# Performance work log

Hardware: AMD Instinct MI355X
Metric: run time of the kernel (lower is better)

Reference implementation:

```python
import jax, jax.numpy as jnp
import numpy as np
from itertools import product

# Static config
B, H, W, C = 16, 64, 64, 256
WIN = 8            # window size (square)
SHIFT = 4          # cyclic shift
NH = 8             # heads
HD = C // NH       # head dim
N = WIN * WIN      # tokens per window
HIDDEN = 1024


def _rel_pos_index():
    coords = np.stack(np.meshgrid(np.arange(WIN), np.arange(WIN), indexing='ij'))  # (2,w,w)
    flat = coords.reshape(2, -1)                                   # (2,N)
    rel = flat[:, :, None] - flat[:, None, :]                      # (2,N,N)
    rel = rel.transpose(1, 2, 0).astype(np.int64)
    rel[..., 0] += WIN - 1
    rel[..., 1] += WIN - 1
    rel[..., 0] *= 2 * WIN - 1
    return rel.sum(-1)                                             # (N,N)


def _shift_mask():
    # additive mask (nW, N, N) with -100 across shift boundaries (generate_mask)
    img = np.zeros((H, W), dtype=np.float32)
    slices = [(slice(0, -WIN), slice(-WIN, -SHIFT), slice(-SHIFT, None))] * 2
    cnt = 0
    for sx, sy in product(*slices):
        img[sx, sy] = cnt
        cnt += 1
    mw = img.reshape(H // WIN, WIN, W // WIN, WIN).transpose(0, 2, 1, 3).reshape(-1, N)  # (nW,N)
    diff = mw[:, None, :] - mw[:, :, None]
    return np.where(diff != 0, -100.0, 0.0).astype(np.float32)     # (nW,N,N)


REL_IDX = jnp.asarray(_rel_pos_index())
MASK = jnp.asarray(_shift_mask())


def _layernorm(x, scale, bias, eps=1e-5):
    mu = jnp.mean(x, axis=-1, keepdims=True)
    var = jnp.mean(jnp.square(x - mu), axis=-1, keepdims=True)
    return (x - mu) * jax.lax.rsqrt(var + eps) * scale + bias


def setup_inputs() -> dict:
    key = jax.random.key(0)
    ks = jax.random.split(key, 8)
    s = lambda fan_in: 1.0 / np.sqrt(fan_in)
    return {
        'x': jax.random.normal(ks[0], (B, H, W, C), jnp.float32),
        'ln1_scale': jnp.ones((C,), jnp.float32),
        'ln1_bias': jnp.zeros((C,), jnp.float32),
        'qkv_w': jax.random.normal(ks[1], (3 * C, C), jnp.float32) * s(C),
        'qkv_b': jnp.zeros((3 * C,), jnp.float32),
        'proj_w': jax.random.normal(ks[2], (C, C), jnp.float32) * s(C),
        'proj_b': jnp.zeros((C,), jnp.float32),
        'rel_bias': jax.random.normal(ks[3], ((2 * WIN - 1) ** 2, NH), jnp.float32) * 0.02,
        'ln2_scale': jnp.ones((C,), jnp.float32),
        'ln2_bias': jnp.zeros((C,), jnp.float32),
        'mlp_w1': jax.random.normal(ks[4], (HIDDEN, C), jnp.float32) * s(C),
        'mlp_b1': jnp.zeros((HIDDEN,), jnp.float32),
        'mlp_w2': jax.random.normal(ks[5], (C, HIDDEN), jnp.float32) * s(HIDDEN),
        'mlp_b2': jnp.zeros((C,), jnp.float32),
    }


def reference(x, ln1_scale, ln1_bias, qkv_w, qkv_b, proj_w, proj_b, rel_bias,
              ln2_scale, ln2_bias, mlp_w1, mlp_b1, mlp_w2, mlp_b2):
    nWh, nWw = H // WIN, W // WIN
    nW = nWh * nWw

    shortcut = x
    h = _layernorm(x, ln1_scale, ln1_bias)
    # cyclic shift
    h = jnp.roll(h, shift=(-SHIFT, -SHIFT), axis=(1, 2))
    # window partition -> (B*nW, N, C)
    h = h.reshape(B, nWh, WIN, nWw, WIN, C).transpose(0, 1, 3, 2, 4, 5).reshape(B * nW, N, C)

    # qkv
    qkv = h @ qkv_w.T + qkv_b                                # (B*nW, N, 3C)
    qkv = qkv.reshape(B * nW, N, 3, NH, HD)
    q, k, v = qkv[:, :, 0], qkv[:, :, 1], qkv[:, :, 2]       # (B*nW, N, NH, HD)

    scale = 1.0 / np.sqrt(HD)
    attn = jnp.einsum('bnhd,bmhd->bhnm', q * scale, k)       # (B*nW, NH, N, N)
    attn = attn + rel_bias[REL_IDX].transpose(2, 0, 1)[None]  # rel-pos bias (NH,N,N)
    attn = attn.reshape(B, nW, NH, N, N) + MASK[None, :, None]
    attn = jax.nn.softmax(attn.reshape(B * nW, NH, N, N), axis=-1)

    out = jnp.einsum('bhnm,bmhd->bnhd', attn, v).reshape(B * nW, N, C)
    out = out @ proj_w.T + proj_b

    # window reverse + reverse shift
    out = out.reshape(B, nWh, nWw, WIN, WIN, C).transpose(0, 1, 3, 2, 4, 5).reshape(B, H, W, C)
    out = jnp.roll(out, shift=(SHIFT, SHIFT), axis=(1, 2))

    x = shortcut + out
    # MLP
    h2 = _layernorm(x, ln2_scale, ln2_bias)
    h2 = jax.nn.gelu(h2 @ mlp_w1.T + mlp_b1, approximate=False) @ mlp_w2.T + mlp_b2
    return x + h2
```

## Files before the change

kernel.cpp:

```cpp
#include <hip/hip_runtime.h>
#include <hip/hip_bf16.h>
#include <math.h>

#define AS1 __attribute__((address_space(1)))
#define AS3 __attribute__((address_space(3)))

typedef __bf16  bf16x8 __attribute__((ext_vector_type(8)));
typedef float   f32x4  __attribute__((ext_vector_type(4)));
typedef __hip_bfloat16 bf16;

__device__ __forceinline__ void gload_lds16(const void* g, void* l) {
  __builtin_amdgcn_global_load_lds((const AS1 void*)g, (AS3 void*)l, 16, 0, 0);
}

__global__ __launch_bounds__(256) void k_conv_weights(
    const float* __restrict__ qkvw, const float* __restrict__ projw,
    const float* __restrict__ w1, const float* __restrict__ w2,
    bf16* __restrict__ dst)
{
  int i = blockIdx.x * 256 + threadIdx.x;
  float v;
  if (i < 196608)       v = qkvw[i];
  else if (i < 262144)  v = projw[i - 196608];
  else if (i < 524288)  v = w1[i - 262144];
  else                  v = w2[i - 524288];
  dst[i] = __float2bfloat16(v);
}

__global__ __launch_bounds__(256) void k_build_btab(
    const float* __restrict__ rel_bias, float* __restrict__ btab)
{
  int i = blockIdx.x * 256 + threadIdx.x;
  int h = i >> 12, r = i & 4095, n = r >> 6, m = r & 63;
  int idx = ((n >> 3) - (m >> 3) + 7) * 15 + ((n & 7) - (m & 7) + 7);
  btab[i] = rel_bias[idx * 8 + h];
}

__global__ __launch_bounds__(256) void k_ln1_window(
    const float* __restrict__ x, const float* __restrict__ sc,
    const float* __restrict__ bi, bf16* __restrict__ hout)
{
  int t = blockIdx.x * 4 + (threadIdx.x >> 6);
  int lane = threadIdx.x & 63;
  int win = t >> 6, nn = t & 63;
  int b = win >> 6, ww = win & 63;
  int ry = ((ww >> 3) << 3) + (nn >> 3);
  int rx = ((ww & 7) << 3) + (nn & 7);
  int sy = (ry + 4) & 63, sx = (rx + 4) & 63;
  const float* src = x + ((size_t)(((b << 6) + sy) << 6) + sx) * 256;
  f32x4 v = *(const f32x4*)(src + lane * 4);
  float s = v[0] + v[1] + v[2] + v[3];
  #pragma unroll
  for (int o = 1; o < 64; o <<= 1) s += __shfl_xor(s, o);
  float mu = s * (1.0f / 256.0f);
  float d0 = v[0]-mu, d1 = v[1]-mu, d2 = v[2]-mu, d3 = v[3]-mu;
  float q = d0*d0 + d1*d1 + d2*d2 + d3*d3;
  #pragma unroll
  for (int o = 1; o < 64; o <<= 1) q += __shfl_xor(q, o);
  float rstd = rsqrtf(q * (1.0f / 256.0f) + 1e-5f);
  int c = lane * 4;
  union { bf16 h[4]; uint2 u; } pk;
  pk.h[0] = __float2bfloat16(d0 * rstd * sc[c+0] + bi[c+0]);
  pk.h[1] = __float2bfloat16(d1 * rstd * sc[c+1] + bi[c+1]);
  pk.h[2] = __float2bfloat16(d2 * rstd * sc[c+2] + bi[c+2]);
  pk.h[3] = __float2bfloat16(d3 * rstd * sc[c+3] + bi[c+3]);
  *(uint2*)(hout + (size_t)t * 256 + c) = pk.u;
}

template<int EPI>
__global__ __launch_bounds__(256, 2) void k_pipe_ar(
    const bf16* __restrict__ A, const bf16* __restrict__ Bw,
    const float* __restrict__ bias,
    float* __restrict__ Cf, bf16* __restrict__ Cb,
    const float* __restrict__ resid,
    const float* __restrict__ ln2s, const float* __restrict__ ln2b,
    bf16* __restrict__ ln2out, int N)
{
  __shared__ __align__(16) char lds[65536 + 10240];

  const int tid = threadIdx.x;
  const int wid = tid >> 6;
  const int lane = tid & 63;
  const int l15 = lane & 15, lh = lane >> 4;
  const int rowBase = blockIdx.x * 128 + wid * 32;
  const int NC = N >> 5;
  char* scr = lds + 65536 + wid * 2560;

  auto stage = [&](int c) {
    char* dst = lds + (c & 3) * 16384;
    const char* srcB = (const char*)Bw + (size_t)c * 32 * 512;
    #pragma unroll
    for (int i = 0; i < 4; ++i) {
      int off = (i * 256 + tid) * 16;
      int r = off >> 9, cb = off & 511;
      int csw = cb ^ ((r & 7) << 4);
      gload_lds16(srcB + (size_t)r * 512 + csw, dst + off);
    }
  };

  bf16x8 af[2][8];
  {
    const bf16* a0 = A + (size_t)(rowBase + l15) * 256 + lh * 8;
    #pragma unroll
    for (int kk = 0; kk < 8; ++kk) {
      af[0][kk] = *(const bf16x8*)(a0 + kk * 32);
      af[1][kk] = *(const bf16x8*)(a0 + 4096 + kk * 32);
    }
  }

  auto remap = [&](int row) -> size_t {
    int win = row >> 6, nn = row & 63;
    int b = win >> 6, ww = win & 63;
    int ry = ((ww >> 3) << 3) + (nn >> 3);
    int rx = ((ww & 7) << 3) + (nn & 7);
    int fy = (ry + 4) & 63, fx = (rx + 4) & 63;
    return ((size_t)(((b << 6) + fy) << 6) + fx) * 256;
  };
  size_t ra0 = 0, ra1 = 0;
  size_t rbA, rbB;
  if (EPI == 2) {
    ra0 = remap(rowBase + l15);
    ra1 = remap(rowBase + 16 + l15);
    rbA = remap(rowBase + (lane >> 2));
    rbB = remap(rowBase + 16 + (lane >> 2));
  } else {
    rbA = (size_t)(rowBase + (lane >> 2)) * N;
    rbB = rbA + (size_t)16 * N;
  }

  const int cl = lh * 4;
  f32x4 bc0 = *(const f32x4*)(bias + cl);
  f32x4 bc1 = *(const f32x4*)(bias + cl + 16);
  f32x4 rc00, rc10, rc01, rc11;
  if (EPI == 2) {
    rc00 = *(const f32x4*)(resid + ra0 + cl);
    rc10 = *(const f32x4*)(resid + ra1 + cl);
    rc01 = *(const f32x4*)(resid + ra0 + cl + 16);
    rc11 = *(const f32x4*)(resid + ra1 + cl + 16);
  }
  stage(0); stage(1); stage(2);
  asm volatile("s_waitcnt vmcnt(8)" ::: "memory");
  __builtin_amdgcn_sched_barrier(0);

  float s0 = 0.f, q0 = 0.f, s1 = 0.f, q1 = 0.f;

  for (int c = 0; c < NC; ++c) {
    __builtin_amdgcn_s_barrier();
    __builtin_amdgcn_sched_barrier(0);

    f32x4 bn0, bn1, rn00, rn10, rn01, rn11;
    if (c + 1 < NC) {
      const int ncl = (c + 1) * 32 + cl;
      bn0 = *(const f32x4*)(bias + ncl);
      bn1 = *(const f32x4*)(bias + ncl + 16);
      if (EPI == 2) {
        rn00 = *(const f32x4*)(resid + ra0 + ncl);
        rn10 = *(const f32x4*)(resid + ra1 + ncl);
        rn01 = *(const f32x4*)(resid + ra0 + ncl + 16);
        rn11 = *(const f32x4*)(resid + ra1 + ncl + 16);
      }
    }
    if (c + 3 < NC) stage(c + 3);

    const char* buf = lds + (c & 3) * 16384;
    const int xr = (l15 & 7) << 4;
    const int base0 = l15 * 512;
    f32x4 a00 = (f32x4){0.f,0.f,0.f,0.f};
    f32x4 a10 = (f32x4){0.f,0.f,0.f,0.f};
    f32x4 a01 = (f32x4){0.f,0.f,0.f,0.f};
    f32x4 a11 = (f32x4){0.f,0.f,0.f,0.f};
    #pragma unroll
    for (int kk = 0; kk < 8; ++kk) {
      const int ko = (kk * 64 + lh * 16) ^ xr;
      bf16x8 b0 = *(const bf16x8*)(buf + base0 + ko);
      bf16x8 b1 = *(const bf16x8*)(buf + base0 + 8192 + ko);
      a00 = __builtin_amdgcn_mfma_f32_16x16x32_bf16(b0, af[0][kk], a00, 0, 0, 0);
      a10 = __builtin_amdgcn_mfma_f32_16x16x32_bf16(b0, af[1][kk], a10, 0, 0, 0);
      a01 = __builtin_amdgcn_mfma_f32_16x16x32_bf16(b1, af[0][kk], a01, 0, 0, 0);
      a11 = __builtin_amdgcn_mfma_f32_16x16x32_bf16(b1, af[1][kk], a11, 0, 0, 0);
    }

    const int cbs = c * 32 + (lane & 3) * 8;
    if (EPI == 0) {
      union { bf16 h[4]; uint2 u; } p00, p01, p10, p11;
      #pragma unroll
      for (int j = 0; j < 4; ++j) {
        p00.h[j] = __float2bfloat16(a00[j] + bc0[j]);
        p01.h[j] = __float2bfloat16(a01[j] + bc1[j]);
        p10.h[j] = __float2bfloat16(a10[j] + bc0[j]);
        p11.h[j] = __float2bfloat16(a11[j] + bc1[j]);
      }
      *(uint2*)(scr + l15 * 80 + lh * 8)            = p00.u;
      *(uint2*)(scr + l15 * 80 + 32 + lh * 8)       = p01.u;
      *(uint2*)(scr + (16 + l15) * 80 + lh * 8)     = p10.u;
      *(uint2*)(scr + (16 + l15) * 80 + 32 + lh * 8)= p11.u;
      uint4 r0 = *(const uint4*)(scr + (lane >> 2) * 80 + (lane & 3) * 16);
      uint4 r1 = *(const uint4*)(scr + (16 + (lane >> 2)) * 80 + (lane & 3) * 16);
      *(uint4*)(Cb + rbA + cbs) = r0;
      *(uint4*)(Cb + rbB + cbs) = r1;
    } else {
      const int colb0 = c * 32 + cl, colb1 = colb0 + 16;
      f32x4 o00, o10, o01, o11;
      #pragma unroll
      for (int j = 0; j < 4; ++j) {
        o00[j] = a00[j] + bc0[j] + rc00[j];
        o10[j] = a10[j] + bc0[j] + rc10[j];
        o01[j] = a01[j] + bc1[j] + rc01[j];
        o11[j] = a11[j] + bc1[j] + rc11[j];
      }
      *(f32x4*)(Cf + ra0 + colb0) = o00;
      *(f32x4*)(Cf + ra1 + colb0) = o10;
      *(f32x4*)(Cf + ra0 + colb1) = o01;
      *(f32x4*)(Cf + ra1 + colb1) = o11;
      #pragma unroll
      for (int j = 0; j < 4; ++j) {
        s0 += o00[j] + o01[j];  q0 += o00[j]*o00[j] + o01[j]*o01[j];
        s1 += o10[j] + o11[j];  q1 += o10[j]*o10[j] + o11[j]*o11[j];
      }
    }

    if (c + 1 < NC) {
      bc0 = bn0; bc1 = bn1;
      if (EPI == 2) { rc00 = rn00; rc10 = rn10; rc01 = rn01; rc11 = rn11; }
    }

    if (c + 1 < NC) {
      if (EPI == 2) {
        if (c == 0)            { asm volatile("s_waitcnt vmcnt(18)" ::: "memory"); }
        else if (c + 3 < NC)   { asm volatile("s_waitcnt vmcnt(28)" ::: "memory"); }
        else                   { asm volatile("s_waitcnt vmcnt(6)"  ::: "memory"); }
      } else {
        if (c == 0)            { asm volatile("s_waitcnt vmcnt(12)" ::: "memory"); }
        else if (c + 3 < NC)   { asm volatile("s_waitcnt vmcnt(16)" ::: "memory"); }
        else                   { asm volatile("s_waitcnt vmcnt(6)"  ::: "memory"); }
      }
      __builtin_amdgcn_sched_barrier(0);
    }
  }

  if (EPI == 2) {
    s0 += __shfl_xor(s0, 16); s0 += __shfl_xor(s0, 32);
    q0 += __shfl_xor(q0, 16); q0 += __shfl_xor(q0, 32);
    s1 += __shfl_xor(s1, 16); s1 += __shfl_xor(s1, 32);
    q1 += __shfl_xor(q1, 16); q1 += __shfl_xor(q1, 32);
    float mu0 = s0 * (1.0f / 256.0f);
    float rs0 = rsqrtf(q0 * (1.0f / 256.0f) - mu0 * mu0 + 1e-5f);
    float mu1 = s1 * (1.0f / 256.0f);
    float rs1 = rsqrtf(q1 * (1.0f / 256.0f) - mu1 * mu1 + 1e-5f);
    for (int c = 0; c < NC; ++c) {
      const int cb0 = c * 32 + cl, cb1 = cb0 + 16;
      f32x4 v00 = *(const f32x4*)(Cf + ra0 + cb0);
      f32x4 v01 = *(const f32x4*)(Cf + ra0 + cb1);
      f32x4 v10 = *(const f32x4*)(Cf + ra1 + cb0);
      f32x4 v11 = *(const f32x4*)(Cf + ra1 + cb1);
      f32x4 sa = *(const f32x4*)(ln2s + cb0);
      f32x4 sb = *(const f32x4*)(ln2s + cb1);
      f32x4 ba = *(const f32x4*)(ln2b + cb0);
      f32x4 bb = *(const f32x4*)(ln2b + cb1);
      union { bf16 h[4]; uint2 u; } p00, p01, p10, p11;
      #pragma unroll
      for (int j = 0; j < 4; ++j) {
        p00.h[j] = __float2bfloat16((v00[j] - mu0) * rs0 * sa[j] + ba[j]);
        p01.h[j] = __float2bfloat16((v01[j] - mu0) * rs0 * sb[j] + bb[j]);
        p10.h[j] = __float2bfloat16((v10[j] - mu1) * rs1 * sa[j] + ba[j]);
        p11.h[j] = __float2bfloat16((v11[j] - mu1) * rs1 * sb[j] + bb[j]);
      }
      *(uint2*)(scr + l15 * 80 + lh * 8)             = p00.u;
      *(uint2*)(scr + l15 * 80 + 32 + lh * 8)        = p01.u;
      *(uint2*)(scr + (16 + l15) * 80 + lh * 8)      = p10.u;
      *(uint2*)(scr + (16 + l15) * 80 + 32 + lh * 8) = p11.u;
      uint4 r0 = *(const uint4*)(scr + (lane >> 2) * 80 + (lane & 3) * 16);
      uint4 r1 = *(const uint4*)(scr + (16 + (lane >> 2)) * 80 + (lane & 3) * 16);
      const int cbs = c * 32 + (lane & 3) * 8;
      *(uint4*)(ln2out + rbA + cbs) = r0;
      *(uint4*)(ln2out + rbB + cbs) = r1;
    }
  }
}

__global__ __launch_bounds__(512, 2) void k_mlp(
    const bf16* __restrict__ A, const bf16* __restrict__ W1,
    const float* __restrict__ B1, const bf16* __restrict__ W2,
    const float* __restrict__ B2, float* __restrict__ X1)
{
  __shared__ __align__(16) char lds[122880];

  const int tid = threadIdx.x;
  const int wid = tid >> 6;
  const int lane = tid & 63;
  const int l15 = lane & 15, lh = lane >> 4;
  const int rowBase = blockIdx.x * 256 + wid * 32;
  char* scr   = lds + 98304 + wid * 2560;
  char* b1lds = lds + 118784;

  auto stage_w1 = [&](int c) {
    char* slot = lds + (c % 3) * 32768;
    const char* srcW1 = (const char*)W1 + (size_t)c * 32 * 512;
    #pragma unroll
    for (int i = 0; i < 2; ++i) {
      int off = (i * 512 + tid) * 16;
      int r = off >> 9, cb = off & 511;
      int csw = cb ^ ((r & 7) << 4);
      gload_lds16(srcW1 + (size_t)r * 512 + csw, slot + off);
    }
  };
  auto stage_w2 = [&](int c) {
    char* dst = lds + ((c + 1) % 3) * 32768 + 16384;
    #pragma unroll
    for (int i = 0; i < 2; ++i) {
      int off = (i * 512 + tid) * 16;
      int ch = off >> 12, row = (off >> 4) & 255;
      gload_lds16((const char*)W2 + (size_t)row * 2048 + (size_t)c * 64 + ch * 16,
                  dst + off);
    }
  };

  if (tid < 256) gload_lds16((const char*)B1 + tid * 16, b1lds + tid * 16);
  bf16x8 af[2][8];
  {
    const bf16* a0 = A + (size_t)(rowBase + l15) * 256 + lh * 8;
    #pragma unroll
    for (int kk = 0; kk < 8; ++kk) {
      af[0][kk] = *(const bf16x8*)(a0 + kk * 32);
      af[1][kk] = *(const bf16x8*)(a0 + 4096 + kk * 32);
    }
  }
  stage_w1(0);
  stage_w1(1);
  stage_w2(0);
  asm volatile("s_waitcnt vmcnt(4)" ::: "memory");
  __builtin_amdgcn_sched_barrier(0);

  f32x4 acc2[2][16];
  #pragma unroll
  for (int m = 0; m < 2; ++m)
    #pragma unroll
    for (int n = 0; n < 16; ++n) acc2[m][n] = (f32x4){0.f,0.f,0.f,0.f};
  bf16x8 actfA = {}, actfB = {};

  for (int c = 0; c < 32; ++c) {
    __builtin_amdgcn_s_barrier();
    __builtin_amdgcn_sched_barrier(0);

    if (c + 2 < 32) stage_w1(c + 2);
    if (c + 1 < 32) stage_w2(c + 1);

    const char* slot  = lds + (c % 3) * 32768;
    const char* w2buf = slot + 16384;
    const int xr = (l15 & 7) << 4;
    const int base0 = l15 * 512;
    const int w2k = lh * 4096;
    f32x4 a00 = (f32x4){0.f,0.f,0.f,0.f};
    f32x4 a10 = (f32x4){0.f,0.f,0.f,0.f};
    f32x4 a01 = (f32x4){0.f,0.f,0.f,0.f};
    f32x4 a11 = (f32x4){0.f,0.f,0.f,0.f};
    if (c > 0) {
      #pragma unroll
      for (int kk = 0; kk < 8; ++kk) {
        const int ko = (kk * 64 + lh * 16) ^ xr;
        bf16x8 b0 = *(const bf16x8*)(slot + base0 + ko);
        bf16x8 b1 = *(const bf16x8*)(slot + base0 + 8192 + ko);
        a00 = __builtin_amdgcn_mfma_f32_16x16x32_bf16(b0, af[0][kk], a00, 0, 0, 0);
        a10 = __builtin_amdgcn_mfma_f32_16x16x32_bf16(b0, af[1][kk], a10, 0, 0, 0);
        a01 = __builtin_amdgcn_mfma_f32_16x16x32_bf16(b1, af[0][kk], a01, 0, 0, 0);
        a11 = __builtin_amdgcn_mfma_f32_16x16x32_bf16(b1, af[1][kk], a11, 0, 0, 0);
        bf16x8 w0 = *(const bf16x8*)(w2buf + w2k + ((2*kk)   * 16 + l15) * 16);
        bf16x8 w1f= *(const bf16x8*)(w2buf + w2k + ((2*kk+1) * 16 + l15) * 16);
        acc2[0][2*kk]   = __builtin_amdgcn_mfma_f32_16x16x32_bf16(w0,  actfA, acc2[0][2*kk],   0, 0, 0);
        acc2[1][2*kk]   = __builtin_amdgcn_mfma_f32_16x16x32_bf16(w0,  actfB, acc2[1][2*kk],   0, 0, 0);
        acc2[0][2*kk+1] = __builtin_amdgcn_mfma_f32_16x16x32_bf16(w1f, actfA, acc2[0][2*kk+1], 0, 0, 0);
        acc2[1][2*kk+1] = __builtin_amdgcn_mfma_f32_16x16x32_bf16(w1f, actfB, acc2[1][2*kk+1], 0, 0, 0);
      }
    } else {
      #pragma unroll
      for (int kk = 0; kk < 8; ++kk) {
        const int ko = (kk * 64 + lh * 16) ^ xr;
        bf16x8 b0 = *(const bf16x8*)(slot + base0 + ko);
        bf16x8 b1 = *(const bf16x8*)(slot + base0 + 8192 + ko);
        a00 = __builtin_amdgcn_mfma_f32_16x16x32_bf16(b0, af[0][kk], a00, 0, 0, 0);
        a10 = __builtin_amdgcn_mfma_f32_16x16x32_bf16(b0, af[1][kk], a10, 0, 0, 0);
        a01 = __builtin_amdgcn_mfma_f32_16x16x32_bf16(b1, af[0][kk], a01, 0, 0, 0);
        a11 = __builtin_amdgcn_mfma_f32_16x16x32_bf16(b1, af[1][kk], a11, 0, 0, 0);
      }
    }

    f32x4 bv0 = *(const f32x4*)(b1lds + c * 128 + lh * 16);
    f32x4 bv1 = *(const f32x4*)(b1lds + c * 128 + 64 + lh * 16);
    auto gelu = [](float v) -> bf16 {
      float w = fmaf(v * v, 0.1029434f, 2.3022083f);
      float e = __builtin_amdgcn_exp2f(-v * w);
      return __float2bfloat16(v * __builtin_amdgcn_rcpf(1.0f + e));
    };
    union { bf16 h[4]; uint2 u; } p00, p01, p10, p11;
    #pragma unroll
    for (int j = 0; j < 4; ++j) {
      p00.h[j] = gelu(a00[j] + bv0[j]);
      p01.h[j] = gelu(a01[j] + bv1[j]);
      p10.h[j] = gelu(a10[j] + bv0[j]);
      p11.h[j] = gelu(a11[j] + bv1[j]);
    }
    *(uint2*)(scr + l15 * 80 + lh * 8)             = p00.u;
    *(uint2*)(scr + l15 * 80 + 32 + lh * 8)        = p01.u;
    *(uint2*)(scr + (16 + l15) * 80 + lh * 8)      = p10.u;
    *(uint2*)(scr + (16 + l15) * 80 + 32 + lh * 8) = p11.u;
    actfA = *(const bf16x8*)(scr + l15 * 80 + lh * 16);
    actfB = *(const bf16x8*)(scr + (16 + l15) * 80 + lh * 16);

    if (c <= 29)      { asm volatile("s_waitcnt vmcnt(4)" ::: "memory"); }
    else if (c == 30) { asm volatile("s_waitcnt vmcnt(2)" ::: "memory"); }
    else              { asm volatile("s_waitcnt vmcnt(0)" ::: "memory"); }
    __builtin_amdgcn_sched_barrier(0);
  }

  __builtin_amdgcn_s_barrier();
  {
    const char* w2buf = lds + 2 * 32768 + 16384;
    const int w2k = lh * 4096;
    #pragma unroll
    for (int n = 0; n < 16; ++n) {
      bf16x8 wf = *(const bf16x8*)(w2buf + w2k + (n * 16 + l15) * 16);
      acc2[0][n] = __builtin_amdgcn_mfma_f32_16x16x32_bf16(wf, actfA, acc2[0][n], 0, 0, 0);
      acc2[1][n] = __builtin_amdgcn_mfma_f32_16x16x32_bf16(wf, actfB, acc2[1][n], 0, 0, 0);
    }
  }

  #pragma unroll
  for (int m = 0; m < 2; ++m) {
    size_t rowAddr = (size_t)(rowBase + m * 16 + l15) * 256;
    #pragma unroll
    for (int n = 0; n < 16; ++n) {
      const int colb = n * 16 + lh * 4;
      const f32x4 b4 = *(const f32x4*)(B2 + colb);
      f32x4* p = (f32x4*)(X1 + rowAddr + colb);
      f32x4 cc = *p;
      #pragma unroll
      for (int j = 0; j < 4; ++j) cc[j] += acc2[m][n][j] + b4[j];
      *p = cc;
    }
  }
}

__global__ __launch_bounds__(256) void k_attn(
    const bf16* __restrict__ qkv, const float* __restrict__ btab,
    bf16* __restrict__ outp)
{
  __shared__ __align__(16) char smem[71680];
  float* sb = (float*)smem;
  const int tid = threadIdx.x, wid = tid >> 6, lane = tid & 63;
  const int l15 = lane & 15, lh = lane >> 4;
  const int h = blockIdx.x >> 8;
  const int win = ((blockIdx.x & 255) << 2) + wid;
  const int tb = win << 6;
  char* plw = smem + 16384 + wid * 9216;
  char* vtw = smem + 16384 + 36864 + wid * 4608;

  for (int i = tid; i < 4096; i += 256) sb[i] = btab[(h << 12) + i];
  __syncthreads();

  bf16x8 qf[4], kf[4];
  #pragma unroll
  for (int m = 0; m < 4; ++m) {
    size_t base = (size_t)(tb + m * 16 + l15) * 768 + h * 32 + lh * 8;
    qf[m] = *(const bf16x8*)(qkv + base);
    kf[m] = *(const bf16x8*)(qkv + base + 256);
  }
  f32x4 s[4][4];
  #pragma unroll
  for (int i = 0; i < 4; ++i)
    #pragma unroll
    for (int j = 0; j < 4; ++j) {
      s[i][j] = (f32x4){0.f,0.f,0.f,0.f};
      s[i][j] = __builtin_amdgcn_mfma_f32_16x16x32_bf16(qf[i], kf[j], s[i][j], 0, 0, 0);
    }

  {
    const bf16* vrow = qkv + (size_t)(tb + lane) * 768 + 512 + h * 32;
    union { uint4 u; bf16 h8[8]; } v0, v1, v2, v3;
    v0.u = *(const uint4*)(vrow);
    v1.u = *(const uint4*)(vrow + 8);
    v2.u = *(const uint4*)(vrow + 16);
    v3.u = *(const uint4*)(vrow + 24);
    #pragma unroll
    for (int j = 0; j < 8; ++j) {
      *(bf16*)(vtw + (j)      * 144 + lane * 2) = v0.h8[j];
      *(bf16*)(vtw + (8 + j)  * 144 + lane * 2) = v1.h8[j];
      *(bf16*)(vtw + (16 + j) * 144 + lane * 2) = v2.h8[j];
      *(bf16*)(vtw + (24 + j) * 144 + lane * 2) = v3.h8[j];
    }
  }

  int ww = win & 63, wi = ww >> 3, wj = ww & 7;
  int labm[4];
  #pragma unroll
  for (int jf = 0; jf < 4; ++jf) {
    int m = jf * 16 + l15;
    int yy = wi * 8 + (m >> 3), xx = wj * 8 + (m & 7);
    labm[jf] = (yy < 56 ? 0 : (yy < 60 ? 1 : 2)) * 3 + (xx < 56 ? 0 : (xx < 60 ? 1 : 2));
  }
  float rsum[4][4];
  const float scale = 0.17677669529663687f;
  #pragma unroll
  for (int i = 0; i < 4; ++i) {
    #pragma unroll
    for (int j = 0; j < 4; ++j) {
      int n = i * 16 + lh * 4 + j;
      int yy = wi * 8 + (n >> 3), xx = wj * 8 + (n & 7);
      int labn = (yy < 56 ? 0 : (yy < 60 ? 1 : 2)) * 3 + (xx < 56 ? 0 : (xx < 60 ? 1 : 2));
      float vals[4]; float mx = -1e30f;
      #pragma unroll
      for (int jf = 0; jf < 4; ++jf) {
        int m = jf * 16 + l15;
        float v = s[i][jf][j] * scale + sb[(n << 6) + m];
        if (labn != labm[jf]) v -= 100.0f;
        vals[jf] = v; mx = fmaxf(mx, v);
      }
      #pragma unroll
      for (int o = 1; o < 16; o <<= 1) mx = fmaxf(mx, __shfl_xor(mx, o));
      float sum = 0.0f;
      #pragma unroll
      for (int jf = 0; jf < 4; ++jf) {
        float e = __expf(vals[jf] - mx);
        sum += e;
        *(bf16*)(plw + n * 144 + (jf * 16 + l15) * 2) = __float2bfloat16(e);
      }
      #pragma unroll
      for (int o = 1; o < 16; o <<= 1) sum += __shfl_xor(sum, o);
      rsum[i][j] = sum;
    }
  }
  __syncthreads();

  f32x4 o[4][2];
  #pragma unroll
  for (int i = 0; i < 4; ++i) { o[i][0] = (f32x4){0.f,0.f,0.f,0.f}; o[i][1] = (f32x4){0.f,0.f,0.f,0.f}; }
  #pragma unroll
  for (int kk = 0; kk < 2; ++kk) {
    bf16x8 pf[4], vf[2];
    #pragma unroll
    for (int i = 0; i < 4; ++i)
      pf[i] = *(const bf16x8*)(plw + (i * 16 + l15) * 144 + kk * 64 + lh * 16);
    #pragma unroll
    for (int df = 0; df < 2; ++df)
      vf[df] = *(const bf16x8*)(vtw + (df * 16 + l15) * 144 + kk * 64 + lh * 16);
    #pragma unroll
    for (int i = 0; i < 4; ++i)
      #pragma unroll
      for (int df = 0; df < 2; ++df)
        o[i][df] = __builtin_amdgcn_mfma_f32_16x16x32_bf16(pf[i], vf[df], o[i][df], 0, 0, 0);
  }
  #pragma unroll
  for (int i = 0; i < 4; ++i)
    #pragma unroll
    for (int df = 0; df < 2; ++df)
      #pragma unroll
      for (int j = 0; j < 4; ++j) {
        int n = i * 16 + lh * 4 + j;
        int d = df * 16 + l15;
        float v = o[i][df][j] / rsum[i][j];
        outp[(size_t)(tb + n) * 256 + h * 32 + d] = __float2bfloat16(v);
      }
}

extern "C" void kernel_launch(void* const* d_in, const int* in_sizes, int n_in,
                              void* d_out, int out_size, void* d_ws, size_t ws_size,
                              hipStream_t stream) {
  (void)in_sizes; (void)n_in; (void)out_size; (void)ws_size;
  const float* x      = (const float*)d_in[0];
  const float* ln1_s  = (const float*)d_in[1];
  const float* ln1_b  = (const float*)d_in[2];
  const float* qkv_w  = (const float*)d_in[3];
  const float* qkv_b  = (const float*)d_in[4];
  const float* proj_w = (const float*)d_in[5];
  const float* proj_b = (const float*)d_in[6];
  const float* rel_b  = (const float*)d_in[7];
  const float* ln2_s  = (const float*)d_in[8];
  const float* ln2_b  = (const float*)d_in[9];
  const float* w1     = (const float*)d_in[10];
  const float* b1     = (const float*)d_in[11];
  const float* w2     = (const float*)d_in[12];
  const float* b2     = (const float*)d_in[13];

  char* ws = (char*)d_ws;
  bf16*  wqkv  = (bf16*)(ws + 0);
  bf16*  wproj = wqkv + 196608;
  bf16*  wm1   = wqkv + 262144;
  bf16*  wm2   = wqkv + 524288;
  float* btab  = (float*)(ws + 1572864);
  bf16*  hbuf  = (bf16*)(ws + 2097152);
  bf16*  qkvb  = (bf16*)(ws + 35651584);
  bf16*  attnb = (bf16*)(ws + 136314880);
  bf16*  ln2buf = hbuf;
  float* x1    = (float*)d_out;

  k_conv_weights<<<3072, 256, 0, stream>>>(qkv_w, proj_w, w1, w2, wqkv);
  k_build_btab<<<128, 256, 0, stream>>>(rel_b, btab);
  k_ln1_window<<<16384, 256, 0, stream>>>(x, ln1_s, ln1_b, hbuf);
  k_pipe_ar<0><<<512, 256, 0, stream>>>(hbuf, wqkv, qkv_b, nullptr, qkvb, nullptr,
                                        nullptr, nullptr, nullptr, 768);
  k_attn<<<2048, 256, 0, stream>>>(qkvb, btab, attnb);
  k_pipe_ar<2><<<512, 256, 0, stream>>>(attnb, wproj, proj_b, x1, nullptr, x,
                                        ln2_s, ln2_b, ln2buf, 256);
  k_mlp<<<256, 512, 0, stream>>>(ln2buf, wm1, b1, wm2, b2, x1);
}
```

Measured before the change: 269.6 us.

## Fuse QKV projection, window attention, output projection and LN2 into one per-window kernel

Replaces the separate QKV GEMM, attention and projection+LN2 kernels with a single kernel that handles one window per block. The window's LN1 output stays in LDS, and Q/K/V, the attention output and the projection result never round-trip through global memory. Weights and bias tables stream through a 3-slot LDS ring per head. This removes large intermediate global writes and reads and two kernel launches. In exchange it uses about 152KB of LDS, which allows only one block per CU, and it re-streams all weights for every window (1024 times), which may make it bound on latency or L2 traffic. LN2 is now computed from bf16-rounded x1 held in LDS, a small change in precision.

```diff
diff --git a/kernel.cpp b/kernel.cpp
--- a/kernel.cpp
+++ b/kernel.cpp
@@ -64,216 +64,304 @@
   pk.h[1] = __float2bfloat16(d1 * rstd * sc[c+1] + bi[c+1]);
   pk.h[2] = __float2bfloat16(d2 * rstd * sc[c+2] + bi[c+2]);
   pk.h[3] = __float2bfloat16(d3 * rstd * sc[c+3] + bi[c+3]);
-  *(uint2*)(hout + (size_t)t * 256 + c) = pk.u;
-}
-
-template<int EPI>
-__global__ __launch_bounds__(256, 2) void k_pipe_ar(
-    const bf16* __restrict__ A, const bf16* __restrict__ Bw,
-    const float* __restrict__ bias,
-    float* __restrict__ Cf, bf16* __restrict__ Cb,
-    const float* __restrict__ resid,
-    const float* __restrict__ ln2s, const float* __restrict__ ln2b,
-    bf16* __restrict__ ln2out, int N)
+  *(uint2*)((char*)hout + (size_t)t * 512 + ((lane * 8) ^ ((t & 7) << 4))) = pk.u;
+}
+
+__global__ __launch_bounds__(256, 1) void k_win(
+    const bf16* __restrict__ hbuf, const bf16* __restrict__ wqkv,
+    const float* __restrict__ qkv_b, const float* __restrict__ btab,
+    const bf16* __restrict__ wproj, const float* __restrict__ proj_b,
+    const float* __restrict__ xres, const float* __restrict__ ln2s,
+    const float* __restrict__ ln2b, float* __restrict__ X1,
+    bf16* __restrict__ ln2out)
 {
-  __shared__ __align__(16) char lds[65536 + 10240];
+  __shared__ __align__(16) char lds[156160];
+  char* ring = lds;
+  char* ldsH = lds + 49152;
+  char* obuf = lds + 81920;
+  char* sbuf = lds + 114688;
+  char* qb   = lds + 131072;
+  char* kb   = lds + 136192;
+  char* vt   = lds + 141312;
+  char* plwA = lds + 145920;
+  float* sums = (float*)(lds + 155136);
 
   const int tid = threadIdx.x;
   const int wid = tid >> 6;
   const int lane = tid & 63;
   const int l15 = lane & 15, lh = lane >> 4;
-  const int rowBase = blockIdx.x * 128 + wid * 32;
-  const int NC = N >> 5;
-  char* scr = lds + 65536 + wid * 2560;
-
-  auto stage = [&](int c) {
-    char* dst = lds + (c & 3) * 16384;
-    const char* srcB = (const char*)Bw + (size_t)c * 32 * 512;
-    #pragma unroll
-    for (int i = 0; i < 4; ++i) {
-      int off = (i * 256 + tid) * 16;
-      int r = off >> 9, cb = off & 511;
-      int csw = cb ^ ((r & 7) << 4);
-      gload_lds16(srcB + (size_t)r * 512 + csw, dst + off);
+  const int wr = (wid >> 1) * 32;
+  const int wn = (wid & 1) * 16;
+  const int win = blockIdx.x;
+  const int tb = win << 6;
+  char* plw = plwA + wid * 2304;
+  const int xr = (l15 & 7) << 4;
+
+  auto stageAt = [&](int i) {
+    if (i < 32 && (i & 3) == 3) {
+      const char* src = (const char*)btab + (size_t)(i >> 2) * 16384;
+      #pragma unroll
+      for (int q = 0; q < 4; ++q) {
+        int off = (q * 256 + tid) * 16;
+        gload_lds16(src + off, sbuf + off);
+      }
+    } else {
+      char* dst = ring + (i % 3) * 16384;
+      const char* wsrc;
+      if (i < 32) { int hh = i >> 2, rr = i & 3;
+                    wsrc = (const char*)(wqkv + (size_t)(rr * 256 + hh * 32) * 256); }
+      else        { wsrc = (const char*)(wproj + (size_t)(i - 32) * 32 * 256); }
+      #pragma unroll
+      for (int q = 0; q < 4; ++q) {
+        int off = (q * 256 + tid) * 16;
+        int rr2 = off >> 9, cb = off & 511;
+        int csw = cb ^ ((rr2 & 7) << 4);
+        gload_lds16(wsrc + (size_t)rr2 * 512 + csw, dst + off);
+      }
     }
   };
 
-  bf16x8 af[2][8];
+  auto remap = [&](int row) -> size_t {
+    int w2 = row >> 6, nn2 = row & 63;
+    int b2 = w2 >> 6, ww3 = w2 & 63;
+    int ry = ((ww3 >> 3) << 3) + (nn2 >> 3);
+    int rx = ((ww3 & 7) << 3) + (nn2 & 7);
+    int fy = (ry + 4) & 63, fx = (rx + 4) & 63;
+    return ((size_t)(((b2 << 6) + fy) << 6) + fx) * 256;
+  };
+
+  f32x4 bcur = *(const f32x4*)(qkv_b + wn + lh * 4);
   {
-    const bf16* a0 = A + (size_t)(rowBase + l15) * 256 + lh * 8;
-    #pragma unroll
-    for (int kk = 0; kk < 8; ++kk) {
-      af[0][kk] = *(const bf16x8*)(a0 + kk * 32);
-      af[1][kk] = *(const bf16x8*)(a0 + 4096 + kk * 32);
-    }
-  }
-
-  auto remap = [&](int row) -> size_t {
-    int win = row >> 6, nn = row & 63;
-    int b = win >> 6, ww = win & 63;
-    int ry = ((ww >> 3) << 3) + (nn >> 3);
-    int rx = ((ww & 7) << 3) + (nn & 7);
-    int fy = (ry + 4) & 63, fx = (rx + 4) & 63;
-    return ((size_t)(((b << 6) + fy) << 6) + fx) * 256;
-  };
-  size_t ra0 = 0, ra1 = 0;
-  size_t rbA, rbB;
-  if (EPI == 2) {
-    ra0 = remap(rowBase + l15);
-    ra1 = remap(rowBase + 16 + l15);
-    rbA = remap(rowBase + (lane >> 2));
-    rbB = remap(rowBase + 16 + (lane >> 2));
-  } else {
-    rbA = (size_t)(rowBase + (lane >> 2)) * N;
-    rbB = rbA + (size_t)16 * N;
-  }
-
-  const int cl = lh * 4;
-  f32x4 bc0 = *(const f32x4*)(bias + cl);
-  f32x4 bc1 = *(const f32x4*)(bias + cl + 16);
-  f32x4 rc00, rc10, rc01, rc11;
-  if (EPI == 2) {
-    rc00 = *(const f32x4*)(resid + ra0 + cl);
-    rc10 = *(const f32x4*)(resid + ra1 + cl);
-    rc01 = *(const f32x4*)(resid + ra0 + cl + 16);
-    rc11 = *(const f32x4*)(resid + ra1 + cl + 16);
-  }
-  stage(0); stage(1); stage(2);
-  asm volatile("s_waitcnt vmcnt(8)" ::: "memory");
+    const char* src = (const char*)hbuf + (size_t)win * 32768;
+    #pragma unroll
+    for (int q = 0; q < 8; ++q) {
+      int off = (q * 256 + tid) * 16;
+      gload_lds16(src + off, ldsH + off);
+    }
+  }
+  stageAt(0);
+  stageAt(1);
+  asm volatile("s_waitcnt vmcnt(4)" ::: "memory");
   __builtin_amdgcn_sched_barrier(0);
 
-  float s0 = 0.f, q0 = 0.f, s1 = 0.f, q1 = 0.f;
-
-  for (int c = 0; c < NC; ++c) {
+  const int ww2 = win & 63, wi2 = ww2 >> 3, wj2 = ww2 & 7;
+  int labm[4];
+  #pragma unroll
+  for (int jf = 0; jf < 4; ++jf) {
+    int m = jf * 16 + l15;
+    int yy = wi2 * 8 + (m >> 3), xx = wj2 * 8 + (m & 7);
+    labm[jf] = (yy < 56 ? 0 : (yy < 60 ? 1 : 2)) * 3 + (xx < 56 ? 0 : (xx < 60 ? 1 : 2));
+  }
+
+  bf16x8 afQ[2][8];
+  f32x4 pbR, rR0, rR1;
+  const size_t pixA0 = remap(tb + wr + l15);
+  const size_t pixA1 = remap(tb + wr + 16 + l15);
+
+  for (int h = 0; h < 8; ++h) {
+    for (int r = 0; r < 3; ++r) {
+      const int p = h * 4 + r;
+      __builtin_amdgcn_s_barrier();
+      __builtin_amdgcn_sched_barrier(0);
+      f32x4 bnext;
+      if (r < 2) bnext = *(const f32x4*)(qkv_b + (r + 1) * 256 + h * 32 + wn + lh * 4);
+      stageAt(p + 2);
+      if (p == 0) {
+        #pragma unroll
+        for (int kk = 0; kk < 8; ++kk) {
+          int rA0 = wr + l15, rA1 = wr + 16 + l15;
+          afQ[0][kk] = *(const bf16x8*)(ldsH + rA0 * 512 + ((lh*16 + kk*64) ^ ((rA0 & 7) << 4)));
+          afQ[1][kk] = *(const bf16x8*)(ldsH + rA1 * 512 + ((lh*16 + kk*64) ^ ((rA1 & 7) << 4)));
+        }
+      }
+      const char* buf = ring + (p % 3) * 16384;
+      f32x4 a0 = (f32x4){0.f,0.f,0.f,0.f};
+      f32x4 a1 = (f32x4){0.f,0.f,0.f,0.f};
+      #pragma unroll
+      for (int kk = 0; kk < 8; ++kk) {
+        bf16x8 wf = *(const bf16x8*)(buf + (wn + l15) * 512 + ((kk*64 + lh*16) ^ xr));
+        a0 = __builtin_amdgcn_mfma_f32_16x16x32_bf16(wf, afQ[0][kk], a0, 0, 0, 0);
+        a1 = __builtin_amdgcn_mfma_f32_16x16x32_bf16(wf, afQ[1][kk], a1, 0, 0, 0);
+      }
+      if (r < 2) {
+        char* dstb = (r == 0) ? qb : kb;
+        union { bf16 hh[4]; uint2 u; } p0, p1;
+        #pragma unroll
+        for (int j = 0; j < 4; ++j) {
+          p0.hh[j] = __float2bfloat16(a0[j] + bcur[j]);
+          p1.hh[j] = __float2bfloat16(a1[j] + bcur[j]);
+        }
+        *(uint2*)(dstb + (wr + l15) * 80 + (wn + lh*4) * 2)      = p0.u;
+        *(uint2*)(dstb + (wr + 16 + l15) * 80 + (wn + lh*4) * 2) = p1.u;
+        bcur = bnext;
+      } else {
+        #pragma unroll
+        for (int j = 0; j < 4; ++j) {
+          *(bf16*)(vt + (wn + lh*4 + j) * 144 + (wr + l15) * 2)      = __float2bfloat16(a0[j] + bcur[j]);
+          *(bf16*)(vt + (wn + lh*4 + j) * 144 + (wr + 16 + l15) * 2) = __float2bfloat16(a1[j] + bcur[j]);
+        }
+      }
+      asm volatile("s_waitcnt vmcnt(4) lgkmcnt(0)" ::: "memory");
+      __builtin_amdgcn_sched_barrier(0);
+    }
+    {
+      const int p = h * 4 + 3;
+      __builtin_amdgcn_s_barrier();
+      __builtin_amdgcn_sched_barrier(0);
+      f32x4 bnext;
+      if (h < 7) bnext = *(const f32x4*)(qkv_b + (h + 1) * 32 + wn + lh * 4);
+      else {
+        pbR = *(const f32x4*)(proj_b + wn + lh * 4);
+        rR0 = *(const f32x4*)(xres + pixA0 + wn + lh * 4);
+        rR1 = *(const f32x4*)(xres + pixA1 + wn + lh * 4);
+      }
+      stageAt(p + 2);
+
+      bf16x8 qf = *(const bf16x8*)(qb + (wid*16 + l15) * 80 + lh * 16);
+      bf16x8 kf[4];
+      f32x4 sj[4];
+      #pragma unroll
+      for (int jf = 0; jf < 4; ++jf) {
+        kf[jf] = *(const bf16x8*)(kb + (jf*16 + l15) * 80 + lh * 16);
+        f32x4 z = (f32x4){0.f,0.f,0.f,0.f};
+        sj[jf] = __builtin_amdgcn_mfma_f32_16x16x32_bf16(qf, kf[jf], z, 0, 0, 0);
+      }
+      const float scale = 0.17677669529663687f;
+      float rsum[4];
+      #pragma unroll
+      for (int j = 0; j < 4; ++j) {
+        int n = wid*16 + lh*4 + j;
+        int yy = wi2*8 + (n >> 3), xx = wj2*8 + (n & 7);
+        int labn = (yy < 56 ? 0 : (yy < 60 ? 1 : 2)) * 3 + (xx < 56 ? 0 : (xx < 60 ? 1 : 2));
+        float vals[4]; float mx = -1e30f;
+        #pragma unroll
+        for (int jf = 0; jf < 4; ++jf) {
+          float v = sj[jf][j] * scale + ((const float*)sbuf)[(n << 6) + jf*16 + l15];
+          if (labn != labm[jf]) v -= 100.0f;
+          vals[jf] = v; mx = fmaxf(mx, v);
+        }
+        #pragma unroll
+        for (int o = 1; o < 16; o <<= 1) mx = fmaxf(mx, __shfl_xor(mx, o));
+        float sum = 0.0f;
+        #pragma unroll
+        for (int jf = 0; jf < 4; ++jf) {
+          float e = __expf(vals[jf] - mx);
+          sum += e;
+          *(bf16*)(plw + (lh*4 + j) * 144 + (jf*16 + l15) * 2) = __float2bfloat16(e);
+        }
+        #pragma unroll
+        for (int o = 1; o < 16; o <<= 1) sum += __shfl_xor(sum, o);
+        rsum[j] = sum;
+      }
+      f32x4 o0 = (f32x4){0.f,0.f,0.f,0.f};
+      f32x4 o1 = (f32x4){0.f,0.f,0.f,0.f};
+      #pragma unroll
+      for (int kk = 0; kk < 2; ++kk) {
+        bf16x8 pf  = *(const bf16x8*)(plw + l15 * 144 + kk*64 + lh*16);
+        bf16x8 vf0 = *(const bf16x8*)(vt + l15 * 144 + kk*64 + lh*16);
+        bf16x8 vf1 = *(const bf16x8*)(vt + (16 + l15) * 144 + kk*64 + lh*16);
+        o0 = __builtin_amdgcn_mfma_f32_16x16x32_bf16(pf, vf0, o0, 0, 0, 0);
+        o1 = __builtin_amdgcn_mfma_f32_16x16x32_bf16(pf, vf1, o1, 0, 0, 0);
+      }
+      #pragma unroll
+      for (int j = 0; j < 4; ++j) {
+        int grow = wid*16 + lh*4 + j;
+        int xg = (grow & 7) << 4;
+        *(bf16*)(obuf + grow*512 + (((h*32 + l15) * 2) ^ xg))      = __float2bfloat16(o0[j] / rsum[j]);
+        *(bf16*)(obuf + grow*512 + (((h*32 + 16 + l15) * 2) ^ xg)) = __float2bfloat16(o1[j] / rsum[j]);
+      }
+      if (h < 7) bcur = bnext;
+      asm volatile("s_waitcnt vmcnt(4) lgkmcnt(0)" ::: "memory");
+      __builtin_amdgcn_sched_barrier(0);
+    }
+  }
+
+  bf16x8 paf[2][8];
+  float ls0 = 0.f, lq0 = 0.f, ls1 = 0.f, lq1 = 0.f;
+  for (int j = 0; j < 8; ++j) {
+    const int p = 32 + j;
     __builtin_amdgcn_s_barrier();
     __builtin_amdgcn_sched_barrier(0);
-
-    f32x4 bn0, bn1, rn00, rn10, rn01, rn11;
-    if (c + 1 < NC) {
-      const int ncl = (c + 1) * 32 + cl;
-      bn0 = *(const f32x4*)(bias + ncl);
-      bn1 = *(const f32x4*)(bias + ncl + 16);
-      if (EPI == 2) {
-        rn00 = *(const f32x4*)(resid + ra0 + ncl);
-        rn10 = *(const f32x4*)(resid + ra1 + ncl);
-        rn01 = *(const f32x4*)(resid + ra0 + ncl + 16);
-        rn11 = *(const f32x4*)(resid + ra1 + ncl + 16);
-      }
-    }
-    if (c + 3 < NC) stage(c + 3);
-
-    const char* buf = lds + (c & 3) * 16384;
-    const int xr = (l15 & 7) << 4;
-    const int base0 = l15 * 512;
-    f32x4 a00 = (f32x4){0.f,0.f,0.f,0.f};
-    f32x4 a10 = (f32x4){0.f,0.f,0.f,0.f};
-    f32x4 a01 = (f32x4){0.f,0.f,0.f,0.f};
-    f32x4 a11 = (f32x4){0.f,0.f,0.f,0.f};
+    f32x4 pbN, rN0, rN1;
+    if (j < 7) {
+      int ncol = (j + 1) * 32 + wn + lh * 4;
+      pbN = *(const f32x4*)(proj_b + ncol);
+      rN0 = *(const f32x4*)(xres + pixA0 + ncol);
+      rN1 = *(const f32x4*)(xres + pixA1 + ncol);
+    }
+    if (p + 2 < 40) stageAt(p + 2);
+    if (j == 0) {
+      #pragma unroll
+      for (int kk = 0; kk < 8; ++kk) {
+        int rA0 = wr + l15, rA1 = wr + 16 + l15;
+        paf[0][kk] = *(const bf16x8*)(obuf + rA0 * 512 + ((lh*16 + kk*64) ^ ((rA0 & 7) << 4)));
+        paf[1][kk] = *(const bf16x8*)(obuf + rA1 * 512 + ((lh*16 + kk*64) ^ ((rA1 & 7) << 4)));
+      }
+    }
+    const char* buf = ring + (p % 3) * 16384;
+    f32x4 a0 = (f32x4){0.f,0.f,0.f,0.f};
+    f32x4 a1 = (f32x4){0.f,0.f,0.f,0.f};
     #pragma unroll
     for (int kk = 0; kk < 8; ++kk) {
-      const int ko = (kk * 64 + lh * 16) ^ xr;
-      bf16x8 b0 = *(const bf16x8*)(buf + base0 + ko);
-      bf16x8 b1 = *(const bf16x8*)(buf + base0 + 8192 + ko);
-      a00 = __builtin_amdgcn_mfma_f32_16x16x32_bf16(b0, af[0][kk], a00, 0, 0, 0);
-      a10 = __builtin_amdgcn_mfma_f32_16x16x32_bf16(b0, af[1][kk], a10, 0, 0, 0);
-      a01 = __builtin_amdgcn_mfma_f32_16x16x32_bf16(b1, af[0][kk], a01, 0, 0, 0);
-      a11 = __builtin_amdgcn_mfma_f32_16x16x32_bf16(b1, af[1][kk], a11, 0, 0, 0);
-    }
-
-    const int cbs = c * 32 + (lane & 3) * 8;
-    if (EPI == 0) {
-      union { bf16 h[4]; uint2 u; } p00, p01, p10, p11;
-      #pragma unroll
-      for (int j = 0; j < 4; ++j) {
-        p00.h[j] = __float2bfloat16(a00[j] + bc0[j]);
-        p01.h[j] = __float2bfloat16(a01[j] + bc1[j]);
-        p10.h[j] = __float2bfloat16(a10[j] + bc0[j]);
-        p11.h[j] = __float2bfloat16(a11[j] + bc1[j]);
-      }
-      *(uint2*)(scr + l15 * 80 + lh * 8)            = p00.u;
-      *(uint2*)(scr + l15 * 80 + 32 + lh * 8)       = p01.u;
-      *(uint2*)(scr + (16 + l15) * 80 + lh * 8)     = p10.u;
-      *(uint2*)(scr + (16 + l15) * 80 + 32 + lh * 8)= p11.u;
-      uint4 r0 = *(const uint4*)(scr + (lane >> 2) * 80 + (lane & 3) * 16);
-      uint4 r1 = *(const uint4*)(scr + (16 + (lane >> 2)) * 80 + (lane & 3) * 16);
-      *(uint4*)(Cb + rbA + cbs) = r0;
-      *(uint4*)(Cb + rbB + cbs) = r1;
-    } else {
-      const int colb0 = c * 32 + cl, colb1 = colb0 + 16;
-      f32x4 o00, o10, o01, o11;
-      #pragma unroll
-      for (int j = 0; j < 4; ++j) {
-        o00[j] = a00[j] + bc0[j] + rc00[j];
-        o10[j] = a10[j] + bc0[j] + rc10[j];
-        o01[j] = a01[j] + bc1[j] + rc01[j];
-        o11[j] = a11[j] + bc1[j] + rc11[j];
-      }
-      *(f32x4*)(Cf + ra0 + colb0) = o00;
-      *(f32x4*)(Cf + ra1 + colb0) = o10;
-      *(f32x4*)(Cf + ra0 + colb1) = o01;
-      *(f32x4*)(Cf + ra1 + colb1) = o11;
-      #pragma unroll
-      for (int j = 0; j < 4; ++j) {
-        s0 += o00[j] + o01[j];  q0 += o00[j]*o00[j] + o01[j]*o01[j];
-        s1 += o10[j] + o11[j];  q1 += o10[j]*o10[j] + o11[j]*o11[j];
-      }
-    }
-
-    if (c + 1 < NC) {
-      bc0 = bn0; bc1 = bn1;
-      if (EPI == 2) { rc00 = rn00; rc10 = rn10; rc01 = rn01; rc11 = rn11; }
-    }
-
-    if (c + 1 < NC) {
-      if (EPI == 2) {
-        if (c == 0)            { asm volatile("s_waitcnt vmcnt(18)" ::: "memory"); }
-        else if (c + 3 < NC)   { asm volatile("s_waitcnt vmcnt(28)" ::: "memory"); }
-        else                   { asm volatile("s_waitcnt vmcnt(6)"  ::: "memory"); }
-      } else {
-        if (c == 0)            { asm volatile("s_waitcnt vmcnt(12)" ::: "memory"); }
-        else if (c + 3 < NC)   { asm volatile("s_waitcnt vmcnt(16)" ::: "memory"); }
-        else                   { asm volatile("s_waitcnt vmcnt(6)"  ::: "memory"); }
-      }
+      bf16x8 wf = *(const bf16x8*)(buf + (wn + l15) * 512 + ((kk*64 + lh*16) ^ xr));
+      a0 = __builtin_amdgcn_mfma_f32_16x16x32_bf16(wf, paf[0][kk], a0, 0, 0, 0);
+      a1 = __builtin_amdgcn_mfma_f32_16x16x32_bf16(wf, paf[1][kk], a1, 0, 0, 0);
+    }
+    const int cloc = j * 32 + wn + lh * 4;
+    f32x4 o0, o1;
+    #pragma unroll
+    for (int jj = 0; jj < 4; ++jj) {
+      o0[jj] = a0[jj] + pbR[jj] + rR0[jj];
+      o1[jj] = a1[jj] + pbR[jj] + rR1[jj];
+      ls0 += o0[jj]; lq0 += o0[jj] * o0[jj];
+      ls1 += o1[jj]; lq1 += o1[jj] * o1[jj];
+    }
+    *(f32x4*)(X1 + pixA0 + cloc) = o0;
+    *(f32x4*)(X1 + pixA1 + cloc) = o1;
+    {
+      union { bf16 hh[4]; uint2 u; } q0, q1;
+      #pragma unroll
+      for (int jj = 0; jj < 4; ++jj) {
+        q0.hh[jj] = __float2bfloat16(o0[jj]);
+        q1.hh[jj] = __float2bfloat16(o1[jj]);
+      }
+      int r0 = wr + l15, r1 = wr + 16 + l15;
+      *(uint2*)(ldsH + r0 * 512 + ((cloc * 2) ^ ((r0 & 7) << 4))) = q0.u;
+      *(uint2*)(ldsH + r1 * 512 + ((cloc * 2) ^ ((r1 & 7) << 4))) = q1.u;
+    }
+    if (j < 7) { pbR = pbN; rR0 = rN0; rR1 = rN1; }
+    if (p < 39) {
+      asm volatile("s_waitcnt vmcnt(4) lgkmcnt(0)" ::: "memory");
       __builtin_amdgcn_sched_barrier(0);
     }
   }
 
-  if (EPI == 2) {
-    s0 += __shfl_xor(s0, 16); s0 += __shfl_xor(s0, 32);
-    q0 += __shfl_xor(q0, 16); q0 += __shfl_xor(q0, 32);
-    s1 += __shfl_xor(s1, 16); s1 += __shfl_xor(s1, 32);
-    q1 += __shfl_xor(q1, 16); q1 += __shfl_xor(q1, 32);
-    float mu0 = s0 * (1.0f / 256.0f);
-    float rs0 = rsqrtf(q0 * (1.0f / 256.0f) - mu0 * mu0 + 1e-5f);
-    float mu1 = s1 * (1.0f / 256.0f);
-    float rs1 = rsqrtf(q1 * (1.0f / 256.0f) - mu1 * mu1 + 1e-5f);
-    for (int c = 0; c < NC; ++c) {
-      const int cb0 = c * 32 + cl, cb1 = cb0 + 16;
-      f32x4 v00 = *(const f32x4*)(Cf + ra0 + cb0);
-      f32x4 v01 = *(const f32x4*)(Cf + ra0 + cb1);
-      f32x4 v10 = *(const f32x4*)(Cf + ra1 + cb0);
-      f32x4 v11 = *(const f32x4*)(Cf + ra1 + cb1);
-      f32x4 sa = *(const f32x4*)(ln2s + cb0);
-      f32x4 sb = *(const f32x4*)(ln2s + cb1);
-      f32x4 ba = *(const f32x4*)(ln2b + cb0);
-      f32x4 bb = *(const f32x4*)(ln2b + cb1);
-      union { bf16 h[4]; uint2 u; } p00, p01, p10, p11;
-      #pragma unroll
-      for (int j = 0; j < 4; ++j) {
-        p00.h[j] = __float2bfloat16((v00[j] - mu0) * rs0 * sa[j] + ba[j]);
-        p01.h[j] = __float2bfloat16((v01[j] - mu0) * rs0 * sb[j] + bb[j]);
-        p10.h[j] = __float2bfloat16((v10[j] - mu1) * rs1 * sa[j] + ba[j]);
-        p11.h[j] = __float2bfloat16((v11[j] - mu1) * rs1 * sb[j] + bb[j]);
-      }
-      *(uint2*)(scr + l15 * 80 + lh * 8)             = p00.u;
-      *(uint2*)(scr + l15 * 80 + 32 + lh * 8)        = p01.u;
-      *(uint2*)(scr + (16 + l15) * 80 + lh * 8)      = p10.u;
-      *(uint2*)(scr + (16 + l15) * 80 + 32 + lh * 8) = p11.u;
-      uint4 r0 = *(const uint4*)(scr + (lane >> 2) * 80 + (lane & 3) * 16);
-      uint4 r1 = *(const uint4*)(scr + (16 + (lane >> 2)) * 80 + (lane & 3) * 16);
-      const int cbs = c * 32 + (lane & 3) * 8;
-      *(uint4*)(ln2out + rbA + cbs) = r0;
-      *(uint4*)(ln2out + rbB + cbs) = r1;
+  ls0 += __shfl_xor(ls0, 16); ls0 += __shfl_xor(ls0, 32);
+  lq0 += __shfl_xor(lq0, 16); lq0 += __shfl_xor(lq0, 32);
+  ls1 += __shfl_xor(ls1, 16); ls1 += __shfl_xor(ls1, 32);
+  lq1 += __shfl_xor(lq1, 16); lq1 += __shfl_xor(lq1, 32);
+  if (lh == 0) {
+    ((float2*)sums)[(wr + l15) * 2 + (wid & 1)]      = make_float2(ls0, lq0);
+    ((float2*)sums)[(wr + 16 + l15) * 2 + (wid & 1)] = make_float2(ls1, lq1);
+  }
+  __syncthreads();
+
+  {
+    f32x4 sR = *(const f32x4*)(ln2s + lane * 4);
+    f32x4 bR = *(const f32x4*)(ln2b + lane * 4);
+    for (int rr = 0; rr < 16; ++rr) {
+      int row = wid * 16 + rr;
+      float2 c0 = ((float2*)sums)[row * 2 + 0];
+      float2 c1 = ((float2*)sums)[row * 2 + 1];
+      float mu = (c0.x + c1.x) * (1.0f / 256.0f);
+      float rs = rsqrtf((c0.y + c1.y) * (1.0f / 256.0f) - mu * mu + 1e-5f);
+      union { uint2 u; bf16 hh[4]; } xin;
+      xin.u = *(const uint2*)(ldsH + row * 512 + ((lane * 8) ^ ((row & 7) << 4)));
+      union { bf16 hh[4]; uint2 u; } pk;
+      #pragma unroll
+      for (int jj = 0; jj < 4; ++jj)
+        pk.hh[jj] = __float2bfloat16((__bfloat162float(xin.hh[jj]) - mu) * rs * sR[jj] + bR[jj]);
+      *(uint2*)(ln2out + remap(tb + row) + lane * 4) = pk.u;
     }
   }
 }
@@ -438,127 +526,6 @@
       *p = cc;
     }
   }
-}
-
-__global__ __launch_bounds__(256) void k_attn(
-    const bf16* __restrict__ qkv, const float* __restrict__ btab,
-    bf16* __restrict__ outp)
-{
-  __shared__ __align__(16) char smem[71680];
-  float* sb = (float*)smem;
-  const int tid = threadIdx.x, wid = tid >> 6, lane = tid & 63;
-  const int l15 = lane & 15, lh = lane >> 4;
-  const int h = blockIdx.x >> 8;
-  const int win = ((blockIdx.x & 255) << 2) + wid;
-  const int tb = win << 6;
-  char* plw = smem + 16384 + wid * 9216;
-  char* vtw = smem + 16384 + 36864 + wid * 4608;
-
-  for (int i = tid; i < 4096; i += 256) sb[i] = btab[(h << 12) + i];
-  __syncthreads();
-
-  bf16x8 qf[4], kf[4];
-  #pragma unroll
-  for (int m = 0; m < 4; ++m) {
-    size_t base = (size_t)(tb + m * 16 + l15) * 768 + h * 32 + lh * 8;
-    qf[m] = *(const bf16x8*)(qkv + base);
-    kf[m] = *(const bf16x8*)(qkv + base + 256);
-  }
-  f32x4 s[4][4];
-  #pragma unroll
-  for (int i = 0; i < 4; ++i)
-    #pragma unroll
-    for (int j = 0; j < 4; ++j) {
-      s[i][j] = (f32x4){0.f,0.f,0.f,0.f};
-      s[i][j] = __builtin_amdgcn_mfma_f32_16x16x32_bf16(qf[i], kf[j], s[i][j], 0, 0, 0);
-    }
-
-  {
-    const bf16* vrow = qkv + (size_t)(tb + lane) * 768 + 512 + h * 32;
-    union { uint4 u; bf16 h8[8]; } v0, v1, v2, v3;
-    v0.u = *(const uint4*)(vrow);
-    v1.u = *(const uint4*)(vrow + 8);
-    v2.u = *(const uint4*)(vrow + 16);
-    v3.u = *(const uint4*)(vrow + 24);
-    #pragma unroll
-    for (int j = 0; j < 8; ++j) {
-      *(bf16*)(vtw + (j)      * 144 + lane * 2) = v0.h8[j];
-      *(bf16*)(vtw + (8 + j)  * 144 + lane * 2) = v1.h8[j];
-      *(bf16*)(vtw + (16 + j) * 144 + lane * 2) = v2.h8[j];
-      *(bf16*)(vtw + (24 + j) * 144 + lane * 2) = v3.h8[j];
-    }
-  }
-
-  int ww = win & 63, wi = ww >> 3, wj = ww & 7;
-  int labm[4];
-  #pragma unroll
-  for (int jf = 0; jf < 4; ++jf) {
-    int m = jf * 16 + l15;
-    int yy = wi * 8 + (m >> 3), xx = wj * 8 + (m & 7);
-    labm[jf] = (yy < 56 ? 0 : (yy < 60 ? 1 : 2)) * 3 + (xx < 56 ? 0 : (xx < 60 ? 1 : 2));
-  }
-  float rsum[4][4];
-  const float scale = 0.17677669529663687f;
-  #pragma unroll
-  for (int i = 0; i < 4; ++i) {
-    #pragma unroll
-    for (int j = 0; j < 4; ++j) {
-      int n = i * 16 + lh * 4 + j;
-      int yy = wi * 8 + (n >> 3), xx = wj * 8 + (n & 7);
-      int labn = (yy < 56 ? 0 : (yy < 60 ? 1 : 2)) * 3 + (xx < 56 ? 0 : (xx < 60 ? 1 : 2));
-      float vals[4]; float mx = -1e30f;
-      #pragma unroll
-      for (int jf = 0; jf < 4; ++jf) {
-        int m = jf * 16 + l15;
-        float v = s[i][jf][j] * scale + sb[(n << 6) + m];
-        if (labn != labm[jf]) v -= 100.0f;
-        vals[jf] = v; mx = fmaxf(mx, v);
-      }
-      #pragma unroll
-      for (int o = 1; o < 16; o <<= 1) mx = fmaxf(mx, __shfl_xor(mx, o));
-      float sum = 0.0f;
-      #pragma unroll
-      for (int jf = 0; jf < 4; ++jf) {
-        float e = __expf(vals[jf] - mx);
-        sum += e;
-        *(bf16*)(plw + n * 144 + (jf * 16 + l15) * 2) = __float2bfloat16(e);
-      }
-      #pragma unroll
-      for (int o = 1; o < 16; o <<= 1) sum += __shfl_xor(sum, o);
-      rsum[i][j] = sum;
-    }
-  }
-  __syncthreads();
-
-  f32x4 o[4][2];
-  #pragma unroll
-  for (int i = 0; i < 4; ++i) { o[i][0] = (f32x4){0.f,0.f,0.f,0.f}; o[i][1] = (f32x4){0.f,0.f,0.f,0.f}; }
-  #pragma unroll
-  for (int kk = 0; kk < 2; ++kk) {
-    bf16x8 pf[4], vf[2];
-    #pragma unroll
-    for (int i = 0; i < 4; ++i)
-      pf[i] = *(const bf16x8*)(plw + (i * 16 + l15) * 144 + kk * 64 + lh * 16);
-    #pragma unroll
-    for (int df = 0; df < 2; ++df)
-      vf[df] = *(const bf16x8*)(vtw + (df * 16 + l15) * 144 + kk * 64 + lh * 16);
-    #pragma unroll
-    for (int i = 0; i < 4; ++i)
-      #pragma unroll
-      for (int df = 0; df < 2; ++df)
-        o[i][df] = __builtin_amdgcn_mfma_f32_16x16x32_bf16(pf[i], vf[df], o[i][df], 0, 0, 0);
-  }
-  #pragma unroll
-  for (int i = 0; i < 4; ++i)
-    #pragma unroll
-    for (int df = 0; df < 2; ++df)
-      #pragma unroll
-      for (int j = 0; j < 4; ++j) {
-        int n = i * 16 + lh * 4 + j;
-        int d = df * 16 + l15;
-        float v = o[i][df][j] / rsum[i][j];
-        outp[(size_t)(tb + n) * 256 + h * 32 + d] = __float2bfloat16(v);
-      }
 }
 
 extern "C" void kernel_launch(void* const* d_in, const int* in_sizes, int n_in,
@@ -587,18 +554,13 @@
   bf16*  wm2   = wqkv + 524288;
   float* btab  = (float*)(ws + 1572864);
   bf16*  hbuf  = (bf16*)(ws + 2097152);
-  bf16*  qkvb  = (bf16*)(ws + 35651584);
-  bf16*  attnb = (bf16*)(ws + 136314880);
-  bf16*  ln2buf = hbuf;
+  bf16*  ln2buf= (bf16*)(ws + 35651584);
   float* x1    = (float*)d_out;
 
   k_conv_weights<<<3072, 256, 0, stream>>>(qkv_w, proj_w, w1, w2, wqkv);
   k_build_btab<<<128, 256, 0, stream>>>(rel_b, btab);
   k_ln1_window<<<16384, 256, 0, stream>>>(x, ln1_s, ln1_b, hbuf);
-  k_pipe_ar<0><<<512, 256, 0, stream>>>(hbuf, wqkv, qkv_b, nullptr, qkvb, nullptr,
-                                        nullptr, nullptr, nullptr, 768);
-  k_attn<<<2048, 256, 0, stream>>>(qkvb, btab, attnb);
-  k_pipe_ar<2><<<512, 256, 0, stream>>>(attnb, wproj, proj_b, x1, nullptr, x,
-                                        ln2_s, ln2_b, ln2buf, 256);
+  k_win<<<1024, 256, 0, stream>>>(hbuf, wqkv, qkv_b, btab, wproj, proj_b,
+                                  x, ln2_s, ln2_b, x1, ln2buf);
   k_mlp<<<256, 512, 0, stream>>>(ln2buf, wm1, b1, wm2, b2, x1);
 }
```

After: 277.7 us. 3.0% more time.
